# Kernel optimization log

Measured on AMD Instinct MI355X. Metric: run time of the kernel, lower is better.

Reference implementation:

```python
import jax, jax.numpy as jnp
import numpy as np

N_EMBD = 1568  # 2 * 784, hard-coded in the source module
HEAD_SIZE = 128
BATCH = 16384


def setup_inputs() -> dict:
    key = jax.random.key(0)
    kx, kq, kk, kv = jax.random.split(key, 4)
    x = jax.random.normal(kx, (BATCH, N_EMBD), dtype=jnp.float32)
    wq = jax.random.normal(kq, (N_EMBD, HEAD_SIZE), dtype=jnp.float32) * (N_EMBD ** -0.5)
    wk = jax.random.normal(kk, (N_EMBD, HEAD_SIZE), dtype=jnp.float32) * (N_EMBD ** -0.5)
    wv = jax.random.normal(kv, (N_EMBD, HEAD_SIZE), dtype=jnp.float32) * (N_EMBD ** -0.5)
    return {"x": x, "wq": wq, "wk": wk, "wv": wv}


def reference(x, wq, wk, wv):
    # x: [B, N]; projections (bias-free Linear): [B, H]
    B, N = x.shape
    q = x @ wq
    k = x @ wk
    v = x @ wv
    # Outer-product score matrix per batch element: [B, H, H]
    attn = jnp.einsum('bi,bj->bij', q, k) * (N ** -0.5)  # scale uses FEATURE dim N, as in source
    attn = jax.nn.softmax(attn, axis=-1)
    # dropout is identity in eval mode
    out = jnp.einsum('bij,bj->bi', attn, v)  # [B, H]
    return out
```

## Files before the change

### kernel.cpp

```cpp
#include <hip/hip_runtime.h>
#include <stdint.h>

typedef unsigned short u16;
typedef __bf16 bf16x8 __attribute__((ext_vector_type(8)));
typedef float f32x4 __attribute__((ext_vector_type(4)));
typedef float f32x2 __attribute__((ext_vector_type(2)));

#define M_ROWS 16384
#define K_DIM  1568
#define H_DIM  128
#define NQ     384
#define MT     32
#define BK     32
#define NSTEP  49
#define NCH    8
#define CHK    6
#define CH_F   192
#define ASTR   200
#define TSTR   40
#define ABUF   (MT * ASTR)
#define PSTR   132
#define KSTRIDE (NQ * BK)
#define SCALE  0.02525381361380526f
#define LOG2E  1.4426950408889634f

__device__ __forceinline__ u16 f32_to_bf16_rne(float f) {
    uint32_t u = __float_as_uint(f);
    uint32_t r = (u + 0x7FFFu + ((u >> 16) & 1u)) >> 16;
    return (u16)r;
}

__device__ __forceinline__ uint32_t cvt_pk(float lo, float hi) {
    uint32_t d;
    asm("v_cvt_pk_bf16_f32 %0, %1, %2" : "=v"(d) : "v"(lo), "v"(hi));
    return d;
}

__device__ __forceinline__ f32x2 pk_mul(f32x2 a, f32x2 b) {
    f32x2 d; asm("v_pk_mul_f32 %0, %1, %2" : "=v"(d) : "v"(a), "v"(b)); return d;
}
__device__ __forceinline__ f32x2 pk_add(f32x2 a, f32x2 b) {
    f32x2 d; asm("v_pk_add_f32 %0, %1, %2" : "=v"(d) : "v"(a), "v"(b)); return d;
}
__device__ __forceinline__ f32x2 pk_fma(f32x2 a, f32x2 b, f32x2 c) {
    f32x2 d; asm("v_pk_fma_f32 %0, %1, %2, %3" : "=v"(d) : "v"(a), "v"(b), "v"(c)); return d;
}

__device__ __forceinline__ void cvt_wr8(u16* dst, f32x4 v) {
    uint2 t; t.x = cvt_pk(v.x, v.y); t.y = cvt_pk(v.z, v.w);
    *(uint2*)dst = t;
}

#define MFMA(a, b, c) __builtin_amdgcn_mfma_f32_16x16x32_bf16(a, b, c, 0, 0, 0)

__global__ __launch_bounds__(256) void wtrans_kernel(
    const float* __restrict__ wq, const float* __restrict__ wk,
    const float* __restrict__ wv, u16* __restrict__ wt2)
{
    __shared__ u16 tile[32][33];
    const float* w = (blockIdx.z == 0) ? wq : (blockIdx.z == 1) ? wk : wv;
    const int k0 = blockIdx.x * 32;
    const int nloc0 = blockIdx.y * 32;
    const int ng0 = blockIdx.z * 128 + nloc0;

    const int tn = threadIdx.x & 31;
    const int tk = threadIdx.x >> 5;
    #pragma unroll
    for (int p = 0; p < 4; p++) {
        int kk = tk + p * 8;
        tile[kk][tn] = f32_to_bf16_rne(w[(size_t)(k0 + kk) * H_DIM + nloc0 + tn]);
    }
    __syncthreads();

    const int klo = threadIdx.x & 31;
    const int tn2 = threadIdx.x >> 5;
    u16* dst = wt2 + (size_t)(k0 >> 5) * KSTRIDE;
    #pragma unroll
    for (int p = 0; p < 4; p++) {
        int nn = tn2 + p * 8;
        dst[(size_t)(ng0 + nn) * 32 + klo] = tile[klo][nn];
    }
}

__global__ __launch_bounds__(512, 4) void fused_kernel(
    const float* __restrict__ x,
    const u16* __restrict__ wt2,
    float* __restrict__ out)
{
    __shared__ char smem[3 * MT * PSTR * 4];
    u16* A0 = (u16*)smem;
    u16* A1 = A0 + ABUF;
    u16* TB = A1 + ABUF;
    float (*Pq)[PSTR] = (float (*)[PSTR])smem;
    float (*Pk)[PSTR] = (float (*)[PSTR])(smem + MT * PSTR * 4);
    float (*Pv)[PSTR] = (float (*)[PSTR])(smem + 2 * MT * PSTR * 4);

    const int tid  = threadIdx.x;
    const int lane = tid & 63;
    const int wave = tid >> 6;
    const int lrow = lane & 15;
    const int quad = lane >> 4;
    const int m0   = blockIdx.x * MT;

    const u16* bp0 = wt2 + (size_t)(wave * 48 +  0 + lrow) * 32 + quad * 8;
    const u16* bp1 = wt2 + (size_t)(wave * 48 + 16 + lrow) * 32 + quad * 8;
    const u16* bp2 = wt2 + (size_t)(wave * 48 + 32 + lrow) * 32 + quad * 8;

    const int srow = tid >> 4;
    const int st16 = tid & 15;
    const float* xrow = x + (size_t)(m0 + srow) * K_DIM;
    u16* wbs[2];
    wbs[0] = A0 + srow * ASTR + st16 * 12;
    wbs[1] = A1 + srow * ASTR + st16 * 12;

    const u16* aF[2][2];
    #pragma unroll
    for (int m = 0; m < 2; m++) {
        aF[0][m] = A0 + (m * 16 + lrow) * ASTR + quad * 8;
        aF[1][m] = A1 + (m * 16 + lrow) * ASTR + quad * 8;
    }

#define LD4(off) (*(const f32x4*)(xrow + (off)))
#define LOADC(S, OFF) do { \
    S[0] = LD4((OFF) + st16 * 12 + 0); \
    S[1] = LD4((OFF) + st16 * 12 + 4); \
    S[2] = LD4((OFF) + st16 * 12 + 8); \
} while (0)
#define WRITEC(WB, S) do { \
    cvt_wr8((WB) + 0, S[0]); cvt_wr8((WB) + 4, S[1]); cvt_wr8((WB) + 8, S[2]); \
} while (0)

    f32x4 acc00 = {}, acc01 = {}, acc02 = {};
    f32x4 acc10 = {}, acc11 = {}, acc12 = {};
    f32x4 sreg[2][3];

    LOADC(sreg[0], 0);
    f32x2 tl = *(const f32x2*)(xrow + 1536 + st16 * 2);
    LOADC(sreg[1], CH_F);
    WRITEC(wbs[0], sreg[0]);
    *(uint32_t*)(TB + srow * TSTR + st16 * 2) = cvt_pk(tl.x, tl.y);

    bf16x8 Ba0 = *(const bf16x8*)(bp0);
    bf16x8 Ba1 = *(const bf16x8*)(bp1);
    bf16x8 Ba2 = *(const bf16x8*)(bp2);
    bf16x8 Bb0 = *(const bf16x8*)(bp0 + KSTRIDE);
    bf16x8 Bb1 = *(const bf16x8*)(bp1 + KSTRIDE);
    bf16x8 Bb2 = *(const bf16x8*)(bp2 + KSTRIDE);
    bf16x8 Bc0 = *(const bf16x8*)(bp0 + 2 * KSTRIDE);
    bf16x8 Bc1 = *(const bf16x8*)(bp1 + 2 * KSTRIDE);
    bf16x8 Bc2 = *(const bf16x8*)(bp2 + 2 * KSTRIDE);
    __syncthreads();

#define KSTEP(AP, IT, G) do { \
    int gp = (G) + 3; if (gp > NSTEP - 1) gp = NSTEP - 1; \
    const size_t o = (size_t)gp * KSTRIDE; \
    bf16x8 Bd0 = *(const bf16x8*)(bp0 + o); \
    bf16x8 Bd1 = *(const bf16x8*)(bp1 + o); \
    bf16x8 Bd2 = *(const bf16x8*)(bp2 + o); \
    bf16x8 a0 = *(const bf16x8*)((AP)[0] + (IT) * BK); \
    bf16x8 a1 = *(const bf16x8*)((AP)[1] + (IT) * BK); \
    acc00 = MFMA(a0, Ba0, acc00); acc10 = MFMA(a1, Ba0, acc10); \
    acc01 = MFMA(a0, Ba1, acc01); acc11 = MFMA(a1, Ba1, acc11); \
    acc02 = MFMA(a0, Ba2, acc02); acc12 = MFMA(a1, Ba2, acc12); \
    Ba0 = Bb0; Ba1 = Bb1; Ba2 = Bb2; \
    Bb0 = Bc0; Bb1 = Bc1; Bb2 = Bc2; \
    Bc0 = Bd0; Bc1 = Bd1; Bc2 = Bd2; \
} while (0)

    #pragma unroll
    for (int c = 0; c < NCH; ++c) {
        if (c < NCH - 1) WRITEC(wbs[(c + 1) & 1], sreg[(c + 1) & 1]);
        if (c < NCH - 2) LOADC(sreg[c & 1], (c + 2) * CH_F);
        #pragma unroll
        for (int it = 0; it < CHK; ++it) KSTEP(aF[c & 1], it, c * CHK + it);
        __syncthreads();
    }

    {
        bf16x8 a0 = *(const bf16x8*)(TB + (lrow +  0) * TSTR + quad * 8);
        bf16x8 a1 = *(const bf16x8*)(TB + (lrow + 16) * TSTR + quad * 8);
        acc00 = MFMA(a0, Ba0, acc00); acc10 = MFMA(a1, Ba0, acc10);
        acc01 = MFMA(a0, Ba1, acc01); acc11 = MFMA(a1, Ba1, acc11);
        acc02 = MFMA(a0, Ba2, acc02); acc12 = MFMA(a1, Ba2, acc12);
    }
    __syncthreads();

#define SCAT(ACC, MTi, NTi) do { \
    const int base = wave * 48 + (NTi) * 16; \
    const int sel  = base >> 7; \
    const int col  = (base & 127) + lrow; \
    const int mrow = (MTi) * 16 + quad * 4; \
    if (sel == 0)      { _Pragma("unroll") for (int rr = 0; rr < 4; rr++) Pq[mrow + rr][col] = ACC[rr] * (SCALE * LOG2E); } \
    else if (sel == 1) { _Pragma("unroll") for (int rr = 0; rr < 4; rr++) Pk[mrow + rr][col] = ACC[rr]; } \
    else               { _Pragma("unroll") for (int rr = 0; rr < 4; rr++) Pv[mrow + rr][col] = ACC[rr]; } \
} while (0)

    SCAT(acc00, 0, 0); SCAT(acc01, 0, 1); SCAT(acc02, 0, 2);
    SCAT(acc10, 1, 0); SCAT(acc11, 1, 1); SCAT(acc12, 1, 2);
    __syncthreads();

    const int r   = tid >> 4;
    const int sub = tid & 15;

    f32x4 qa = *(const f32x4*)&Pq[r][sub * 8];
    f32x4 qb = *(const f32x4*)&Pq[r][sub * 8 + 4];
    f32x2 qp0; qp0.x = qa.x; qp0.y = qa.y;
    f32x2 qp1; qp1.x = qa.z; qp1.y = qa.w;
    f32x2 qp2; qp2.x = qb.x; qp2.y = qb.y;
    f32x2 qp3; qp3.x = qb.z; qp3.y = qb.w;

    f32x2 d0 = {}, d1 = {}, d2 = {}, d3 = {};
    f32x2 n0 = {}, n1 = {}, n2 = {}, n3 = {};

    #pragma unroll 4
    for (int j4 = 0; j4 < 32; ++j4) {
        f32x4 k4 = *(const f32x4*)&Pk[r][j4 * 4];
        f32x4 v4 = *(const f32x4*)&Pv[r][j4 * 4];
        #pragma unroll
        for (int jj = 0; jj < 4; ++jj) {
            float kj = k4[jj];
            float vj = v4[jj];
            f32x2 kk; kk.x = kj; kk.y = kj;
            f32x2 vv; vv.x = vj; vv.y = vj;
            f32x2 s0 = pk_mul(qp0, kk);
            f32x2 s1 = pk_mul(qp1, kk);
            f32x2 s2 = pk_mul(qp2, kk);
            f32x2 s3 = pk_mul(qp3, kk);
            f32x2 e0; e0.x = __builtin_amdgcn_exp2f(s0.x); e0.y = __builtin_amdgcn_exp2f(s0.y);
            f32x2 e1; e1.x = __builtin_amdgcn_exp2f(s1.x); e1.y = __builtin_amdgcn_exp2f(s1.y);
            f32x2 e2; e2.x = __builtin_amdgcn_exp2f(s2.x); e2.y = __builtin_amdgcn_exp2f(s2.y);
            f32x2 e3; e3.x = __builtin_amdgcn_exp2f(s3.x); e3.y = __builtin_amdgcn_exp2f(s3.y);
            d0 = pk_add(d0, e0); n0 = pk_fma(e0, vv, n0);
            d1 = pk_add(d1, e1); n1 = pk_fma(e1, vv, n1);
            d2 = pk_add(d2, e2); n2 = pk_fma(e2, vv, n2);
            d3 = pk_add(d3, e3); n3 = pk_fma(e3, vv, n3);
        }
    }

    float* op = out + (size_t)(m0 + r) * H_DIM + sub * 8;
    f32x4 o0, o1;
    o0.x = n0.x / d0.x; o0.y = n0.y / d0.y; o0.z = n1.x / d1.x; o0.w = n1.y / d1.y;
    o1.x = n2.x / d2.x; o1.y = n2.y / d2.y; o1.z = n3.x / d3.x; o1.w = n3.y / d3.y;
    __builtin_nontemporal_store(o0, (f32x4*)(op));
    __builtin_nontemporal_store(o1, (f32x4*)(op + 4));
}

extern "C" void kernel_launch(void* const* d_in, const int* in_sizes, int n_in,
                              void* d_out, int out_size, void* d_ws, size_t ws_size,
                              hipStream_t stream)
{
    const float* x  = (const float*)d_in[0];
    const float* wq = (const float*)d_in[1];
    const float* wk = (const float*)d_in[2];
    const float* wv = (const float*)d_in[3];
    float* out = (float*)d_out;

    u16* wt2 = (u16*)d_ws;

    wtrans_kernel<<<dim3(K_DIM / 32, H_DIM / 32, 3), 256, 0, stream>>>(wq, wk, wv, wt2);
    fused_kernel<<<M_ROWS / MT, 512, 0, stream>>>(x, wt2, out);
}
```

Baseline: 205.2 us.

## Load x fragments directly from global into MFMA registers, drop LDS staging

Removes the LDS double-buffered staging of x (chunked loads, bf16 convert, shared writes, per-chunk barriers). Each wave now loads its own A fragments straight from global memory, converts them to bf16 in registers, and feeds the MFMAs, with a simple unrolled loop over the 49 K-steps. This cuts shared-memory traffic and synchronization. In exchange, all 8 waves load the same x rows redundantly from global/L2, and the explicit B-operand prefetch pipeline is gone, leaving latency hiding to the compiler and occupancy.

```diff
diff --git a/kernel.cpp b/kernel.cpp
--- a/kernel.cpp
+++ b/kernel.cpp
@@ -2,6 +2,7 @@
 #include <stdint.h>
 
 typedef unsigned short u16;
+typedef uint32_t u32;
 typedef __bf16 bf16x8 __attribute__((ext_vector_type(8)));
 typedef float f32x4 __attribute__((ext_vector_type(4)));
 typedef float f32x2 __attribute__((ext_vector_type(2)));
@@ -11,31 +12,20 @@
 #define H_DIM  128
 #define NQ     384
 #define MT     32
-#define BK     32
 #define NSTEP  49
-#define NCH    8
-#define CHK    6
-#define CH_F   192
-#define ASTR   200
-#define TSTR   40
-#define ABUF   (MT * ASTR)
+#define KSTRIDE (NQ * 32)
 #define PSTR   132
-#define KSTRIDE (NQ * BK)
 #define SCALE  0.02525381361380526f
 #define LOG2E  1.4426950408889634f
 
 __device__ __forceinline__ u16 f32_to_bf16_rne(float f) {
-    uint32_t u = __float_as_uint(f);
-    uint32_t r = (u + 0x7FFFu + ((u >> 16) & 1u)) >> 16;
+    u32 u = __float_as_uint(f);
+    u32 r = (u + 0x7FFFu + ((u >> 16) & 1u)) >> 16;
     return (u16)r;
 }
-
-__device__ __forceinline__ uint32_t cvt_pk(float lo, float hi) {
-    uint32_t d;
-    asm("v_cvt_pk_bf16_f32 %0, %1, %2" : "=v"(d) : "v"(lo), "v"(hi));
-    return d;
+__device__ __forceinline__ u32 cvt_pk(float lo, float hi) {
+    u32 d; asm("v_cvt_pk_bf16_f32 %0, %1, %2" : "=v"(d) : "v"(lo), "v"(hi)); return d;
 }
-
 __device__ __forceinline__ f32x2 pk_mul(f32x2 a, f32x2 b) {
     f32x2 d; asm("v_pk_mul_f32 %0, %1, %2" : "=v"(d) : "v"(a), "v"(b)); return d;
 }
@@ -45,10 +35,11 @@
 __device__ __forceinline__ f32x2 pk_fma(f32x2 a, f32x2 b, f32x2 c) {
     f32x2 d; asm("v_pk_fma_f32 %0, %1, %2, %3" : "=v"(d) : "v"(a), "v"(b), "v"(c)); return d;
 }
-
-__device__ __forceinline__ void cvt_wr8(u16* dst, f32x4 v) {
-    uint2 t; t.x = cvt_pk(v.x, v.y); t.y = cvt_pk(v.z, v.w);
-    *(uint2*)dst = t;
+__device__ __forceinline__ bf16x8 pack_bf16(f32x4 a, f32x4 b) {
+    union { u32 u[4]; bf16x8 v; } r;
+    r.u[0] = cvt_pk(a.x, a.y); r.u[1] = cvt_pk(a.z, a.w);
+    r.u[2] = cvt_pk(b.x, b.y); r.u[3] = cvt_pk(b.z, b.w);
+    return r.v;
 }
 
 #define MFMA(a, b, c) __builtin_amdgcn_mfma_f32_16x16x32_bf16(a, b, c, 0, 0, 0)
@@ -88,9 +79,6 @@
     float* __restrict__ out)
 {
     __shared__ char smem[3 * MT * PSTR * 4];
-    u16* A0 = (u16*)smem;
-    u16* A1 = A0 + ABUF;
-    u16* TB = A1 + ABUF;
     float (*Pq)[PSTR] = (float (*)[PSTR])smem;
     float (*Pk)[PSTR] = (float (*)[PSTR])(smem + MT * PSTR * 4);
     float (*Pv)[PSTR] = (float (*)[PSTR])(smem + 2 * MT * PSTR * 4);
@@ -106,84 +94,28 @@
     const u16* bp1 = wt2 + (size_t)(wave * 48 + 16 + lrow) * 32 + quad * 8;
     const u16* bp2 = wt2 + (size_t)(wave * 48 + 32 + lrow) * 32 + quad * 8;
 
-    const int srow = tid >> 4;
-    const int st16 = tid & 15;
-    const float* xrow = x + (size_t)(m0 + srow) * K_DIM;
-    u16* wbs[2];
-    wbs[0] = A0 + srow * ASTR + st16 * 12;
-    wbs[1] = A1 + srow * ASTR + st16 * 12;
-
-    const u16* aF[2][2];
-    #pragma unroll
-    for (int m = 0; m < 2; m++) {
-        aF[0][m] = A0 + (m * 16 + lrow) * ASTR + quad * 8;
-        aF[1][m] = A1 + (m * 16 + lrow) * ASTR + quad * 8;
-    }
-
-#define LD4(off) (*(const f32x4*)(xrow + (off)))
-#define LOADC(S, OFF) do { \
-    S[0] = LD4((OFF) + st16 * 12 + 0); \
-    S[1] = LD4((OFF) + st16 * 12 + 4); \
-    S[2] = LD4((OFF) + st16 * 12 + 8); \
-} while (0)
-#define WRITEC(WB, S) do { \
-    cvt_wr8((WB) + 0, S[0]); cvt_wr8((WB) + 4, S[1]); cvt_wr8((WB) + 8, S[2]); \
-} while (0)
+    const float* xr0 = x + (size_t)(m0 + lrow)      * K_DIM + quad * 8;
+    const float* xr1 = x + (size_t)(m0 + 16 + lrow) * K_DIM + quad * 8;
 
     f32x4 acc00 = {}, acc01 = {}, acc02 = {};
     f32x4 acc10 = {}, acc11 = {}, acc12 = {};
-    f32x4 sreg[2][3];
 
-    LOADC(sreg[0], 0);
-    f32x2 tl = *(const f32x2*)(xrow + 1536 + st16 * 2);
-    LOADC(sreg[1], CH_F);
-    WRITEC(wbs[0], sreg[0]);
-    *(uint32_t*)(TB + srow * TSTR + st16 * 2) = cvt_pk(tl.x, tl.y);
-
-    bf16x8 Ba0 = *(const bf16x8*)(bp0);
-    bf16x8 Ba1 = *(const bf16x8*)(bp1);
-    bf16x8 Ba2 = *(const bf16x8*)(bp2);
-    bf16x8 Bb0 = *(const bf16x8*)(bp0 + KSTRIDE);
-    bf16x8 Bb1 = *(const bf16x8*)(bp1 + KSTRIDE);
-    bf16x8 Bb2 = *(const bf16x8*)(bp2 + KSTRIDE);
-    bf16x8 Bc0 = *(const bf16x8*)(bp0 + 2 * KSTRIDE);
-    bf16x8 Bc1 = *(const bf16x8*)(bp1 + 2 * KSTRIDE);
-    bf16x8 Bc2 = *(const bf16x8*)(bp2 + 2 * KSTRIDE);
-    __syncthreads();
-
-#define KSTEP(AP, IT, G) do { \
-    int gp = (G) + 3; if (gp > NSTEP - 1) gp = NSTEP - 1; \
-    const size_t o = (size_t)gp * KSTRIDE; \
-    bf16x8 Bd0 = *(const bf16x8*)(bp0 + o); \
-    bf16x8 Bd1 = *(const bf16x8*)(bp1 + o); \
-    bf16x8 Bd2 = *(const bf16x8*)(bp2 + o); \
-    bf16x8 a0 = *(const bf16x8*)((AP)[0] + (IT) * BK); \
-    bf16x8 a1 = *(const bf16x8*)((AP)[1] + (IT) * BK); \
-    acc00 = MFMA(a0, Ba0, acc00); acc10 = MFMA(a1, Ba0, acc10); \
-    acc01 = MFMA(a0, Ba1, acc01); acc11 = MFMA(a1, Ba1, acc11); \
-    acc02 = MFMA(a0, Ba2, acc02); acc12 = MFMA(a1, Ba2, acc12); \
-    Ba0 = Bb0; Ba1 = Bb1; Ba2 = Bb2; \
-    Bb0 = Bc0; Bb1 = Bc1; Bb2 = Bc2; \
-    Bc0 = Bd0; Bc1 = Bd1; Bc2 = Bd2; \
-} while (0)
-
-    #pragma unroll
-    for (int c = 0; c < NCH; ++c) {
-        if (c < NCH - 1) WRITEC(wbs[(c + 1) & 1], sreg[(c + 1) & 1]);
-        if (c < NCH - 2) LOADC(sreg[c & 1], (c + 2) * CH_F);
-        #pragma unroll
-        for (int it = 0; it < CHK; ++it) KSTEP(aF[c & 1], it, c * CHK + it);
-        __syncthreads();
+    #pragma unroll 7
+    for (int g = 0; g < NSTEP; ++g) {
+        f32x4 a0lo = *(const f32x4*)(xr0 + g * 32);
+        f32x4 a0hi = *(const f32x4*)(xr0 + g * 32 + 4);
+        f32x4 a1lo = *(const f32x4*)(xr1 + g * 32);
+        f32x4 a1hi = *(const f32x4*)(xr1 + g * 32 + 4);
+        const size_t o = (size_t)g * KSTRIDE;
+        bf16x8 b0 = *(const bf16x8*)(bp0 + o);
+        bf16x8 b1 = *(const bf16x8*)(bp1 + o);
+        bf16x8 b2 = *(const bf16x8*)(bp2 + o);
+        bf16x8 a0 = pack_bf16(a0lo, a0hi);
+        bf16x8 a1 = pack_bf16(a1lo, a1hi);
+        acc00 = MFMA(a0, b0, acc00); acc10 = MFMA(a1, b0, acc10);
+        acc01 = MFMA(a0, b1, acc01); acc11 = MFMA(a1, b1, acc11);
+        acc02 = MFMA(a0, b2, acc02); acc12 = MFMA(a1, b2, acc12);
     }
-
-    {
-        bf16x8 a0 = *(const bf16x8*)(TB + (lrow +  0) * TSTR + quad * 8);
-        bf16x8 a1 = *(const bf16x8*)(TB + (lrow + 16) * TSTR + quad * 8);
-        acc00 = MFMA(a0, Ba0, acc00); acc10 = MFMA(a1, Ba0, acc10);
-        acc01 = MFMA(a0, Ba1, acc01); acc11 = MFMA(a1, Ba1, acc11);
-        acc02 = MFMA(a0, Ba2, acc02); acc12 = MFMA(a1, Ba2, acc12);
-    }
-    __syncthreads();
 
 #define SCAT(ACC, MTi, NTi) do { \
     const int base = wave * 48 + (NTi) * 16; \
```

New measurement: 270.8 us. 1.32x slower.
